# Performance work log

Measured on AMD Instinct MI355X. Metric: run time of the kernel, lower is better.

The kernel has to match this reference:

```python
import jax, jax.numpy as jnp
import numpy as np
from jax import lax

B, Hh, Ww, DIM = 8, 32, 32, 768
NH, NP = 6, 4
DV = int(DIM * 0.5)        # value dim (deform_ratio=0.5) = 384
DH = DV // NH              # per-head dim = 64
HID = int(DIM * 0.25)      # ConvFFN hidden = 192
N_TOK = 21 * (Hh * Ww // 4)  # 5376 query tokens (3-level pyramid)
LIN = Hh * Ww              # 1024 feat tokens (single level)
EPS = 1e-6


def _ln(x, g, b):
    mu = jnp.mean(x, -1, keepdims=True)
    var = jnp.mean((x - mu) ** 2, -1, keepdims=True)
    return (x - mu) * lax.rsqrt(var + EPS) * g + b


def _bilinear(value, loc, h, w):
    # value: (B, h*w, NH, DH); loc: (B, Lq, NH, NP, 2) normalized (x, y) in [0,1]
    # grid_sample semantics: align_corners=False, zero padding
    x = loc[..., 0] * w - 0.5
    y = loc[..., 1] * h - 0.5
    x0 = jnp.floor(x)
    y0 = jnp.floor(y)
    wx = x - x0
    wy = y - y0
    b, lq, nh, p = x.shape
    out = jnp.zeros((b, lq, nh, p, value.shape[-1]), value.dtype)
    for dy, wyy in ((0, 1.0 - wy), (1, wy)):
        for dx, wxx in ((0, 1.0 - wx), (1, wx)):
            xi = x0 + dx
            yi = y0 + dy
            valid = (xi >= 0) & (xi < w) & (yi >= 0) & (yi < h)
            xi_c = jnp.clip(xi, 0, w - 1).astype(jnp.int32)
            yi_c = jnp.clip(yi, 0, h - 1).astype(jnp.int32)
            idx = yi_c * w + xi_c                          # (B,Lq,NH,NP)
            idx = idx.transpose(0, 1, 3, 2).reshape(b, lq * p, nh)
            g = jnp.take_along_axis(value, idx[..., None], axis=1)  # (B,Lq*P,NH,DH)
            g = g.reshape(b, lq, p, nh, -1).transpose(0, 1, 3, 2, 4)
            out = out + g * (wxx * wyy * valid.astype(value.dtype))[..., None]
    return out


def setup_inputs() -> dict:
    key = jax.random.key(0)
    ks = jax.random.split(key, 24)
    s = 0.02
    inp = {
        'query': jax.random.normal(ks[0], (B, N_TOK, DIM), jnp.float32),
        'reference_points': jax.random.uniform(ks[1], (B, N_TOK, 1, 2), jnp.float32),
        'feat': jax.random.normal(ks[2], (B, LIN, DIM), jnp.float32),
        'spatial_shapes': jnp.array([[Hh, Ww]], jnp.int32),
        'level_start_index': jnp.zeros((1,), jnp.int32),
        'qn_g': jnp.ones((DIM,), jnp.float32),
        'qn_b': jnp.zeros((DIM,), jnp.float32),
        'fn_g': jnp.ones((DIM,), jnp.float32),
        'fn_b': jnp.zeros((DIM,), jnp.float32),
        'W_off': jax.random.normal(ks[3], (DIM, NH * NP * 2), jnp.float32) * s,
        'b_off': jax.random.normal(ks[4], (NH * NP * 2,), jnp.float32) * s,
        'W_attn': jax.random.normal(ks[5], (DIM, NH * NP), jnp.float32) * s,
        'b_attn': jnp.zeros((NH * NP,), jnp.float32),
        'W_val': jax.random.normal(ks[6], (DIM, DV), jnp.float32) * s,
        'b_val': jnp.zeros((DV,), jnp.float32),
        'W_out': jax.random.normal(ks[7], (DV, DIM), jnp.float32) * s,
        'b_out': jnp.zeros((DIM,), jnp.float32),
        'ffn_g': jnp.ones((DIM,), jnp.float32),
        'ffn_b': jnp.zeros((DIM,), jnp.float32),
        'fc1_w': jax.random.normal(ks[8], (DIM, HID), jnp.float32) * s,
        'fc1_b': jnp.zeros((HID,), jnp.float32),
        'dw_w': jax.random.normal(ks[9], (3, 3, 1, HID), jnp.float32) * s,  # HWIO depthwise
        'dw_b': jnp.zeros((HID,), jnp.float32),
        'fc2_w': jax.random.normal(ks[10], (HID, DIM), jnp.float32) * s,
        'fc2_b': jnp.zeros((DIM,), jnp.float32),
        'h': Hh,
        'w': Ww,
    }
    return inp


def reference(query, reference_points, feat, spatial_shapes, level_start_index,
              qn_g, qn_b, fn_g, fn_b, W_off, b_off, W_attn, b_attn, W_val, b_val,
              W_out, b_out, ffn_g, ffn_b, fc1_w, fc1_b, dw_w, dw_b, fc2_w, fc2_b,
              h, w):
    b, lq, _ = query.shape
    # ---- MSDeformAttn (single level) ----
    q = _ln(query, qn_g, qn_b)
    v = _ln(feat, fn_g, fn_b) @ W_val + b_val            # (B, LIN, DV)
    v = v.reshape(b, -1, NH, DH)
    off = (q @ W_off + b_off).reshape(b, lq, NH, 1, NP, 2)
    aw = jax.nn.softmax((q @ W_attn + b_attn).reshape(b, lq, NH, NP), axis=-1)
    normalizer = jnp.array([w, h], q.dtype)              # (W, H) for x,y offsets
    loc = reference_points[:, :, None, :, None, :] + off / normalizer  # (B,Lq,NH,1,NP,2)
    sampled = _bilinear(v, loc[:, :, :, 0], h, w)        # (B,Lq,NH,NP,DH)
    attn = jnp.einsum('blhpd,blhp->blhd', sampled, aw).reshape(b, lq, DV)
    attn = attn @ W_out + b_out
    x = query + attn
    # ---- ConvFFN residual ----
    y = _ln(x, ffn_g, ffn_b) @ fc1_w + fc1_b             # (B, N, HID)
    n = lq // 21
    def dw(z, hh, ww):
        z = z.reshape(b, hh, ww, HID)
        z = lax.conv_general_dilated(z, dw_w, (1, 1), 'SAME',
                                     dimension_numbers=('NHWC', 'HWIO', 'NHWC'),
                                     feature_group_count=HID) + dw_b
        return z.reshape(b, hh * ww, HID)
    y = jnp.concatenate([dw(y[:, :16 * n], 2 * h, 2 * w),
                         dw(y[:, 16 * n:20 * n], h, w),
                         dw(y[:, 20 * n:], h // 2, w // 2)], axis=1)
    y = jax.nn.gelu(y, approximate=False)
    y = y @ fc2_w + fc2_b
    return x + y
```

## Files before the change

kernel.cpp:

```cpp
#include <hip/hip_runtime.h>
#include <hip/hip_bf16.h>
#include <math.h>

#define B_    8
#define DIM_  768
#define NH_   6
#define NP_   4
#define DV_   384
#define DH_   64
#define HID_  192
#define NTOK_ 5376
#define LIN_  1024
#define HH_   32
#define WW_   32
#define MQ_   (B_ * NTOK_)
#define MF_   (B_ * LIN_)

using fv4  = __attribute__((ext_vector_type(4))) float;
using bfv8 = __attribute__((ext_vector_type(8))) __bf16;
using sv8  = __attribute__((ext_vector_type(8))) short;
using sv4  = __attribute__((ext_vector_type(4))) short;

__device__ __forceinline__ short f2bf(float f) {
  union { float f; unsigned u; } v; v.f = f;
  unsigned r = v.u + 0x7FFFu + ((v.u >> 16) & 1u);
  return (short)(r >> 16);
}
__device__ __forceinline__ float bf2f(short s) {
  union { unsigned u; float f; } v;
  v.u = ((unsigned)(unsigned short)s) << 16;
  return v.f;
}

__device__ __forceinline__ void gload16(const short* g, short* l) {
  __builtin_amdgcn_global_load_lds(
      (const __attribute__((address_space(1))) void*)g,
      (__attribute__((address_space(3))) void*)l, 16, 0, 0);
}

__device__ __forceinline__ float block_sum_f(float v, float* red, int nwaves) {
#pragma unroll
  for (int o = 32; o > 0; o >>= 1) v += __shfl_down(v, o, 64);
  int wid = threadIdx.x >> 6;
  int lane = threadIdx.x & 63;
  if (lane == 0) red[wid] = v;
  __syncthreads();
  float s = 0.f;
  for (int i = 0; i < nwaves; ++i) s += red[i];
  __syncthreads();
  return s;
}

__global__ __launch_bounds__(256) void ln_apply(const float* __restrict__ X,
                                                const float* __restrict__ g,
                                                const float* __restrict__ b,
                                                short* __restrict__ Y) {
  __shared__ float red[4];
  const int row = blockIdx.x;
  const float* xr = X + (size_t)row * DIM_;
  const int t = threadIdx.x;
  float x0 = xr[t], x1 = xr[t + 256], x2 = xr[t + 512];
  float s = block_sum_f(x0 + x1 + x2, red, 4);
  const float m = s * (1.f / 768.f);
  float d0 = x0 - m, d1 = x1 - m, d2 = x2 - m;
  float sq = block_sum_f(d0 * d0 + d1 * d1 + d2 * d2, red, 4);
  const float rs = rsqrtf(sq * (1.f / 768.f) + 1e-6f);
  short* yr = Y + (size_t)row * DIM_;
  yr[t]       = f2bf(d0 * rs * g[t]       + b[t]);
  yr[t + 256] = f2bf(d1 * rs * g[t + 256] + b[t + 256]);
  yr[t + 512] = f2bf(d2 * rs * g[t + 512] + b[t + 512]);
}

__global__ __launch_bounds__(256) void tconv(const float* __restrict__ src,
                                             short* __restrict__ dst,
                                             int K, int N, int rowOff) {
  const int i = blockIdx.x * 256 + threadIdx.x;
  if (i >= K * N) return;
  const int n = i / K, k = i % K;
  dst[(size_t)(n + rowOff) * K + k] = f2bf(src[(size_t)k * N + n]);
}

__global__ __launch_bounds__(256) void zfill(short* __restrict__ p, int n) {
  const int i = blockIdx.x * 256 + threadIdx.x;
  if (i < n) p[i] = 0;
}

template <int NT>
__global__ __launch_bounds__(256) void gemm_mfma(
    const short* __restrict__ A, const short* __restrict__ Bt,
    const float* __restrict__ bias, const float* __restrict__ addend,
    float* __restrict__ C, short* __restrict__ Cb,
    int M, int N, int K) {
  __shared__ short As[2][8192];
  __shared__ short Bs[2][8192];

  const int bid = blockIdx.x;
  const int xcd = bid & 7;
  const int slot = bid >> 3;
  const int mpx = (M >> 7) >> 3;
  const int mt = xcd * mpx + slot / NT;
  const int nt = slot % NT;
  const int bm = mt << 7;
  const int bn = nt << 7;

  const int t = threadIdx.x;
  const int lane = t & 63;
  const int wid = t >> 6;
  const int wr = (wid >> 1) * 64;
  const int wc = (wid & 1) * 64;
  const int l15 = lane & 15;
  const int l4 = lane >> 4;
  const int lr = lane >> 3;
  const int cs = ((((lane & 7) << 4) ^ (lr << 4)) >> 1);
  const int xorv = (l15 & 7) << 4;

  const short* pa0 = A + (size_t)(bm + wid * 32 + lr) * K + cs;
  const short* pb0 = Bt + (size_t)(bn + wid * 32 + lr) * K + cs;
  short* la0 = &As[0][wid * 2048];
  short* lb0 = &Bs[0][wid * 2048];
  short* la1 = &As[1][wid * 2048];
  short* lb1 = &Bs[1][wid * 2048];

  auto stage = [&](int buf, int kt) {
    const short* pa = pa0 + kt;
    const short* pb = pb0 + kt;
    short* la = buf ? la1 : la0;
    short* lb = buf ? lb1 : lb0;
#pragma unroll
    for (int i = 0; i < 4; ++i) {
      gload16(pa + (size_t)i * 8 * K, la + i * 512);
      gload16(pb + (size_t)i * 8 * K, lb + i * 512);
    }
  };

  fv4 acc[4][4] = {};
  const int nsteps = K >> 6;
  int cur = 0;
  stage(0, 0);
  __syncthreads();

  for (int tstep = 0; tstep < nsteps; ++tstep) {
    if (tstep + 1 < nsteps) stage(cur ^ 1, (tstep + 1) << 6);
    const short* Ab = As[cur];
    const short* Bb = Bs[cur];
#pragma unroll
    for (int kk = 0; kk < 2; ++kk) {
      const int cb = (l4 << 4) + (kk << 6);
      const int co = (cb ^ xorv) >> 1;
      bfv8 af[4], bfr[4];
#pragma unroll
      for (int m = 0; m < 4; ++m)
        af[m] = *(const bfv8*)&Ab[((wr + m * 16 + l15) << 6) + co];
#pragma unroll
      for (int n = 0; n < 4; ++n)
        bfr[n] = *(const bfv8*)&Bb[((wc + n * 16 + l15) << 6) + co];
#pragma unroll
      for (int m = 0; m < 4; ++m)
#pragma unroll
        for (int n = 0; n < 4; ++n)
          acc[m][n] = __builtin_amdgcn_mfma_f32_16x16x32_bf16(
              bfr[n], af[m], acc[m][n], 0, 0, 0);
    }
    __syncthreads();
    cur ^= 1;
  }

  const int rb = bm + wr + l15;
  const int cbase = bn + wc + l4 * 4;
#pragma unroll
  for (int n = 0; n < 4; ++n) {
    const int colb = cbase + n * 16;
    if (colb >= N) continue;
    fv4 bv = {};
    if (bias) bv = *(const fv4*)&bias[colb];
#pragma unroll
    for (int m = 0; m < 4; ++m) {
      const int row = rb + m * 16;
      const size_t o = (size_t)row * N + colb;
      fv4 vv = acc[m][n] + bv;
      if (addend) vv += *(const fv4*)&addend[o];
      if (C) {
        *(fv4*)&C[o] = vv;
      } else {
        sv4 r;
        r[0] = f2bf(vv[0]); r[1] = f2bf(vv[1]);
        r[2] = f2bf(vv[2]); r[3] = f2bf(vv[3]);
        *(sv4*)&Cb[o] = r;
      }
    }
  }
}

__global__ __launch_bounds__(256) void prep_taps(
    const float* __restrict__ ref, const float* __restrict__ boff,
    const float* __restrict__ battn, const float* __restrict__ oa,
    int* __restrict__ taps) {
  const int i = blockIdx.x * 256 + threadIdx.x;
  if (i >= MQ_ * NH_) return;
  const int row = i / NH_, head = i % NH_;
  const float rx = ref[(size_t)row * 2 + 0];
  const float ry = ref[(size_t)row * 2 + 1];
  const float* o = oa + (size_t)row * 72 + head * 8;
  const float* ap = oa + (size_t)row * 72 + 48 + head * 4;
  float l0 = ap[0] + battn[head * 4 + 0];
  float l1 = ap[1] + battn[head * 4 + 1];
  float l2 = ap[2] + battn[head * 4 + 2];
  float l3 = ap[3] + battn[head * 4 + 3];
  float mx = fmaxf(fmaxf(l0, l1), fmaxf(l2, l3));
  float e0 = expf(l0 - mx), e1 = expf(l1 - mx);
  float e2 = expf(l2 - mx), e3 = expf(l3 - mx);
  float sinv = 1.f / (e0 + e1 + e2 + e3);
  float aw[4] = {e0 * sinv, e1 * sinv, e2 * sinv, e3 * sinv};

  int st[32];
  int k = 0;
#pragma unroll
  for (int p = 0; p < 4; ++p) {
    const float lx = rx + (o[p * 2 + 0] + boff[head * 8 + p * 2 + 0]) * (1.f / 32.f);
    const float ly = ry + (o[p * 2 + 1] + boff[head * 8 + p * 2 + 1]) * (1.f / 32.f);
    const float x = lx * (float)WW_ - 0.5f;
    const float y = ly * (float)HH_ - 0.5f;
    const float x0f = floorf(x), y0f = floorf(y);
    const float wx = x - x0f, wy = y - y0f;
    const int x0 = (int)x0f, y0 = (int)y0f;
    const float a = aw[p];
#pragma unroll
    for (int dy = 0; dy < 2; ++dy) {
      const int yi = y0 + dy;
      const float wyy = dy ? wy : 1.f - wy;
#pragma unroll
      for (int dx = 0; dx < 2; ++dx) {
        const int xi = x0 + dx;
        const float wxx = dx ? wx : 1.f - wx;
        const bool valid = ((unsigned)xi < (unsigned)WW_) & ((unsigned)yi < (unsigned)HH_);
        const int xc = min(max(xi, 0), WW_ - 1);
        const int yc = min(max(yi, 0), HH_ - 1);
        st[k++] = (yc * WW_ + xc) * DV_;
        float w = a * wxx * wyy;
        st[k++] = __float_as_int(valid ? w : 0.f);
      }
    }
  }
  int4* dst = (int4*)(taps + (size_t)i * 32);
#pragma unroll
  for (int j = 0; j < 8; ++j)
    dst[j] = make_int4(st[4 * j], st[4 * j + 1], st[4 * j + 2], st[4 * j + 3]);
}

__global__ __launch_bounds__(256) void msda_sample2(const short* __restrict__ v,
                                                    const int* __restrict__ taps,
                                                    short* __restrict__ outv) {
  const int gid = blockIdx.x * 256 + threadIdx.x;
  const int pair = gid >> 4;
  const int ch0 = (gid & 15) * 4;
  const int row = pair / NH_;
  const int head = pair - row * NH_;
  const int b = row / NTOK_;
  const short* vb = v + (size_t)b * LIN_ * DV_ + head * DH_ + ch0;
  const int4* tp = (const int4*)(taps + (size_t)pair * 32);
  float a0 = 0.f, a1 = 0.f, a2 = 0.f, a3 = 0.f;
#pragma unroll
  for (int j = 0; j < 8; ++j) {
    int4 pr = tp[j];
    {
      sv4 val = *(const sv4*)&vb[pr.x];
      const float w = __int_as_float(pr.y);
      a0 += w * bf2f(val[0]); a1 += w * bf2f(val[1]);
      a2 += w * bf2f(val[2]); a3 += w * bf2f(val[3]);
    }
    {
      sv4 val = *(const sv4*)&vb[pr.z];
      const float w = __int_as_float(pr.w);
      a0 += w * bf2f(val[0]); a1 += w * bf2f(val[1]);
      a2 += w * bf2f(val[2]); a3 += w * bf2f(val[3]);
    }
  }
  sv4 r;
  r[0] = f2bf(a0); r[1] = f2bf(a1); r[2] = f2bf(a2); r[3] = f2bf(a3);
  *(sv4*)&outv[(size_t)gid * 4] = r;
}

__global__ __launch_bounds__(256) void conv_gelu(const short* __restrict__ y1,
                                                 const float* __restrict__ dww,
                                                 const float* __restrict__ dwb,
                                                 short* __restrict__ y2) {
  const int i = blockIdx.x * 256 + threadIdx.x;
  if (i >= B_ * NTOK_ * HID_) return;
  const int c = i % HID_;
  const int tmp = i / HID_;
  const int tok = tmp % NTOK_;
  const int b = tmp / NTOK_;
  int base, LH, LW;
  if (tok < 4096)      { base = 0;    LH = 64; LW = 64; }
  else if (tok < 5120) { base = 4096; LH = 32; LW = 32; }
  else                 { base = 5120; LH = 16; LW = 16; }
  const int pos = tok - base;
  const int hh = pos / LW, ww = pos % LW;
  float z = dwb[c];
  const short* yb = y1 + ((size_t)b * NTOK_ + base) * HID_ + c;
#pragma unroll
  for (int ky = 0; ky < 3; ++ky) {
    const int yy = hh + ky - 1;
    if ((unsigned)yy >= (unsigned)LH) continue;
#pragma unroll
    for (int kx = 0; kx < 3; ++kx) {
      const int xx = ww + kx - 1;
      if ((unsigned)xx >= (unsigned)LW) continue;
      z += bf2f(yb[(size_t)(yy * LW + xx) * HID_]) * dww[(ky * 3 + kx) * HID_ + c];
    }
  }
  y2[i] = f2bf(0.5f * z * (1.f + erff(z * 0.70710678118654752f)));
}

extern "C" void kernel_launch(void* const* d_in, const int* in_sizes, int n_in,
                              void* d_out, int out_size, void* d_ws, size_t ws_size,
                              hipStream_t stream) {
  const float* query  = (const float*)d_in[0];
  const float* ref    = (const float*)d_in[1];
  const float* feat   = (const float*)d_in[2];
  const float* qn_g   = (const float*)d_in[5];
  const float* qn_b   = (const float*)d_in[6];
  const float* fn_g   = (const float*)d_in[7];
  const float* fn_b   = (const float*)d_in[8];
  const float* W_off  = (const float*)d_in[9];
  const float* b_off  = (const float*)d_in[10];
  const float* W_attn = (const float*)d_in[11];
  const float* b_attn = (const float*)d_in[12];
  const float* W_val  = (const float*)d_in[13];
  const float* b_val  = (const float*)d_in[14];
  const float* W_out  = (const float*)d_in[15];
  const float* b_out  = (const float*)d_in[16];
  const float* ffn_g  = (const float*)d_in[17];
  const float* ffn_b  = (const float*)d_in[18];
  const float* fc1_w  = (const float*)d_in[19];
  const float* fc1_b  = (const float*)d_in[20];
  const float* dw_w   = (const float*)d_in[21];
  const float* dw_b   = (const float*)d_in[22];
  const float* fc2_w  = (const float*)d_in[23];
  const float* fc2_b  = (const float*)d_in[24];
  float* out = (float*)d_out;
  char* wsb = (char*)d_ws;

  short* qn_xn = (short*)(wsb + 0);
  int*   taps  = (int*)(wsb + 0);
  short* vbf   = (short*)(wsb + 66060288);
  float* oa    = (float*)(wsb + 72351744);
  short* attnv = (short*)(wsb + 84738048);
  short* y1b   = (short*)(wsb + 84738048);
  short* fnb   = (short*)(wsb + 117768192);
  short* y2    = (short*)(wsb + 117768192);
  short* oat   = (short*)(wsb + 130351104);
  short* vt    = (short*)(wsb + 134283264);
  short* ot    = (short*)(wsb + 134873088);
  short* f1t   = (short*)(wsb + 135462912);
  short* f2t   = (short*)(wsb + 135757824);

  zfill<<<(128 * 768 + 255) / 256, 256, 0, stream>>>(oat, 128 * 768);
  tconv<<<(768 * 384 + 255) / 256, 256, 0, stream>>>(W_val, vt, 768, 384, 0);
  tconv<<<(768 * 48 + 255) / 256, 256, 0, stream>>>(W_off, oat, 768, 48, 0);
  tconv<<<(768 * 24 + 255) / 256, 256, 0, stream>>>(W_attn, oat, 768, 24, 48);
  tconv<<<(384 * 768 + 255) / 256, 256, 0, stream>>>(W_out, ot, 384, 768, 0);
  tconv<<<(768 * 192 + 255) / 256, 256, 0, stream>>>(fc1_w, f1t, 768, 192, 0);
  tconv<<<(192 * 768 + 255) / 256, 256, 0, stream>>>(fc2_w, f2t, 192, 768, 0);

  ln_apply<<<MQ_, 256, 0, stream>>>(query, qn_g, qn_b, qn_xn);
  ln_apply<<<MF_, 256, 0, stream>>>(feat, fn_g, fn_b, fnb);

  gemm_mfma<3><<<(MF_ / 128) * 3, 256, 0, stream>>>(
      fnb, vt, b_val, nullptr, nullptr, vbf, MF_, 384, 768);

  gemm_mfma<1><<<(MQ_ / 128) * 1, 256, 0, stream>>>(
      qn_xn, oat, nullptr, nullptr, oa, nullptr, MQ_, 72, 768);

  prep_taps<<<(MQ_ * NH_ + 255) / 256, 256, 0, stream>>>(ref, b_off, b_attn, oa, taps);

  msda_sample2<<<MQ_ * NH_ * 16 / 256, 256, 0, stream>>>(vbf, taps, attnv);

  gemm_mfma<6><<<(MQ_ / 128) * 6, 256, 0, stream>>>(
      attnv, ot, b_out, query, out, nullptr, MQ_, 768, 384);

  ln_apply<<<MQ_, 256, 0, stream>>>(out, ffn_g, ffn_b, qn_xn);

  gemm_mfma<2><<<(MQ_ / 128) * 2, 256, 0, stream>>>(
      qn_xn, f1t, fc1_b, nullptr, nullptr, y1b, MQ_, 192, 768);

  conv_gelu<<<(MQ_ * HID_ + 255) / 256, 256, 0, stream>>>(y1b, dw_w, dw_b, y2);

  gemm_mfma<6><<<(MQ_ / 128) * 6, 256, 0, stream>>>(
      y2, f2t, fc2_b, out, out, nullptr, MQ_, 768, 192);
}
```

Before: 705.7 us.

## Shrink GEMM tiles to 64x64 and vectorize LayerNorm with 192 threads

The MFMA GEMM block tile drops from 128x128 to 64x64, each wave now owning 32x32 with 2x2 accumulators, and the LDS staging is reworked to match. Grids grow roughly fourfold, which raises occupancy and spreads small-N GEMMs over more CUs. The cost is lower arithmetic intensity per block, since each block reloads more A/B data per output. LayerNorm also moves to 192 threads, each loading one float4, storing four bf16 values in one write, and reading gamma and beta as vectors.

```diff
diff --git a/kernel.cpp b/kernel.cpp
--- a/kernel.cpp
+++ b/kernel.cpp
@@ -51,24 +51,28 @@
   return s;
 }
 
-__global__ __launch_bounds__(256) void ln_apply(const float* __restrict__ X,
+__global__ __launch_bounds__(192) void ln_apply(const float* __restrict__ X,
                                                 const float* __restrict__ g,
                                                 const float* __restrict__ b,
                                                 short* __restrict__ Y) {
-  __shared__ float red[4];
+  __shared__ float red[3];
   const int row = blockIdx.x;
-  const float* xr = X + (size_t)row * DIM_;
   const int t = threadIdx.x;
-  float x0 = xr[t], x1 = xr[t + 256], x2 = xr[t + 512];
-  float s = block_sum_f(x0 + x1 + x2, red, 4);
+  const fv4 x = ((const fv4*)(X + (size_t)row * DIM_))[t];
+  float s = block_sum_f(x[0] + x[1] + x[2] + x[3], red, 3);
   const float m = s * (1.f / 768.f);
-  float d0 = x0 - m, d1 = x1 - m, d2 = x2 - m;
-  float sq = block_sum_f(d0 * d0 + d1 * d1 + d2 * d2, red, 4);
+  fv4 d = x - m;
+  float sq = block_sum_f(d[0] * d[0] + d[1] * d[1] + d[2] * d[2] + d[3] * d[3],
+                         red, 3);
   const float rs = rsqrtf(sq * (1.f / 768.f) + 1e-6f);
-  short* yr = Y + (size_t)row * DIM_;
-  yr[t]       = f2bf(d0 * rs * g[t]       + b[t]);
-  yr[t + 256] = f2bf(d1 * rs * g[t + 256] + b[t + 256]);
-  yr[t + 512] = f2bf(d2 * rs * g[t + 512] + b[t + 512]);
+  const fv4 g4 = ((const fv4*)g)[t];
+  const fv4 b4 = ((const fv4*)b)[t];
+  sv4 r;
+  r[0] = f2bf(d[0] * rs * g4[0] + b4[0]);
+  r[1] = f2bf(d[1] * rs * g4[1] + b4[1]);
+  r[2] = f2bf(d[2] * rs * g4[2] + b4[2]);
+  r[3] = f2bf(d[3] * rs * g4[3] + b4[3]);
+  ((sv4*)(Y + (size_t)row * DIM_))[t] = r;
 }
 
 __global__ __launch_bounds__(256) void tconv(const float* __restrict__ src,
@@ -91,49 +95,45 @@
     const float* __restrict__ bias, const float* __restrict__ addend,
     float* __restrict__ C, short* __restrict__ Cb,
     int M, int N, int K) {
-  __shared__ short As[2][8192];
-  __shared__ short Bs[2][8192];
+  __shared__ short As[2][4096];
+  __shared__ short Bs[2][4096];
 
   const int bid = blockIdx.x;
   const int xcd = bid & 7;
   const int slot = bid >> 3;
-  const int mpx = (M >> 7) >> 3;
+  const int mpx = (M >> 6) >> 3;
   const int mt = xcd * mpx + slot / NT;
   const int nt = slot % NT;
-  const int bm = mt << 7;
-  const int bn = nt << 7;
+  const int bm = mt << 6;
+  const int bn = nt << 6;
 
   const int t = threadIdx.x;
   const int lane = t & 63;
   const int wid = t >> 6;
-  const int wr = (wid >> 1) * 64;
-  const int wc = (wid & 1) * 64;
+  const int wr = (wid >> 1) * 32;
+  const int wc = (wid & 1) * 32;
   const int l15 = lane & 15;
   const int l4 = lane >> 4;
   const int lr = lane >> 3;
   const int cs = ((((lane & 7) << 4) ^ (lr << 4)) >> 1);
   const int xorv = (l15 & 7) << 4;
 
-  const short* pa0 = A + (size_t)(bm + wid * 32 + lr) * K + cs;
-  const short* pb0 = Bt + (size_t)(bn + wid * 32 + lr) * K + cs;
-  short* la0 = &As[0][wid * 2048];
-  short* lb0 = &Bs[0][wid * 2048];
-  short* la1 = &As[1][wid * 2048];
-  short* lb1 = &Bs[1][wid * 2048];
+  const short* pa0 = A + (size_t)(bm + wid * 8 + lr) * K + cs;
+  const short* pb0 = Bt + (size_t)(bn + wid * 8 + lr) * K + cs;
 
   auto stage = [&](int buf, int kt) {
     const short* pa = pa0 + kt;
     const short* pb = pb0 + kt;
-    short* la = buf ? la1 : la0;
-    short* lb = buf ? lb1 : lb0;
-#pragma unroll
-    for (int i = 0; i < 4; ++i) {
-      gload16(pa + (size_t)i * 8 * K, la + i * 512);
-      gload16(pb + (size_t)i * 8 * K, lb + i * 512);
+    short* la = &As[buf][wid * 512];
+    short* lb = &Bs[buf][wid * 512];
+#pragma unroll
+    for (int i = 0; i < 2; ++i) {
+      gload16(pa + (size_t)(i * 32) * K, la + i * 2048);
+      gload16(pb + (size_t)(i * 32) * K, lb + i * 2048);
     }
   };
 
-  fv4 acc[4][4] = {};
+  fv4 acc[2][2] = {};
   const int nsteps = K >> 6;
   int cur = 0;
   stage(0, 0);
@@ -147,17 +147,17 @@
     for (int kk = 0; kk < 2; ++kk) {
       const int cb = (l4 << 4) + (kk << 6);
       const int co = (cb ^ xorv) >> 1;
-      bfv8 af[4], bfr[4];
-#pragma unroll
-      for (int m = 0; m < 4; ++m)
+      bfv8 af[2], bfr[2];
+#pragma unroll
+      for (int m = 0; m < 2; ++m)
         af[m] = *(const bfv8*)&Ab[((wr + m * 16 + l15) << 6) + co];
 #pragma unroll
-      for (int n = 0; n < 4; ++n)
+      for (int n = 0; n < 2; ++n)
         bfr[n] = *(const bfv8*)&Bb[((wc + n * 16 + l15) << 6) + co];
 #pragma unroll
-      for (int m = 0; m < 4; ++m)
-#pragma unroll
-        for (int n = 0; n < 4; ++n)
+      for (int m = 0; m < 2; ++m)
+#pragma unroll
+        for (int n = 0; n < 2; ++n)
           acc[m][n] = __builtin_amdgcn_mfma_f32_16x16x32_bf16(
               bfr[n], af[m], acc[m][n], 0, 0, 0);
     }
@@ -168,13 +168,13 @@
   const int rb = bm + wr + l15;
   const int cbase = bn + wc + l4 * 4;
 #pragma unroll
-  for (int n = 0; n < 4; ++n) {
+  for (int n = 0; n < 2; ++n) {
     const int colb = cbase + n * 16;
     if (colb >= N) continue;
     fv4 bv = {};
     if (bias) bv = *(const fv4*)&bias[colb];
 #pragma unroll
-    for (int m = 0; m < 4; ++m) {
+    for (int m = 0; m < 2; ++m) {
       const int row = rb + m * 16;
       const size_t o = (size_t)row * N + colb;
       fv4 vv = acc[m][n] + bv;
@@ -363,29 +363,29 @@
   tconv<<<(768 * 192 + 255) / 256, 256, 0, stream>>>(fc1_w, f1t, 768, 192, 0);
   tconv<<<(192 * 768 + 255) / 256, 256, 0, stream>>>(fc2_w, f2t, 192, 768, 0);
 
-  ln_apply<<<MQ_, 256, 0, stream>>>(query, qn_g, qn_b, qn_xn);
-  ln_apply<<<MF_, 256, 0, stream>>>(feat, fn_g, fn_b, fnb);
-
-  gemm_mfma<3><<<(MF_ / 128) * 3, 256, 0, stream>>>(
+  ln_apply<<<MQ_, 192, 0, stream>>>(query, qn_g, qn_b, qn_xn);
+  ln_apply<<<MF_, 192, 0, stream>>>(feat, fn_g, fn_b, fnb);
+
+  gemm_mfma<6><<<(MF_ / 64) * 6, 256, 0, stream>>>(
       fnb, vt, b_val, nullptr, nullptr, vbf, MF_, 384, 768);
 
-  gemm_mfma<1><<<(MQ_ / 128) * 1, 256, 0, stream>>>(
+  gemm_mfma<2><<<(MQ_ / 64) * 2, 256, 0, stream>>>(
       qn_xn, oat, nullptr, nullptr, oa, nullptr, MQ_, 72, 768);
 
   prep_taps<<<(MQ_ * NH_ + 255) / 256, 256, 0, stream>>>(ref, b_off, b_attn, oa, taps);
 
   msda_sample2<<<MQ_ * NH_ * 16 / 256, 256, 0, stream>>>(vbf, taps, attnv);
 
-  gemm_mfma<6><<<(MQ_ / 128) * 6, 256, 0, stream>>>(
+  gemm_mfma<12><<<(MQ_ / 64) * 12, 256, 0, stream>>>(
       attnv, ot, b_out, query, out, nullptr, MQ_, 768, 384);
 
-  ln_apply<<<MQ_, 256, 0, stream>>>(out, ffn_g, ffn_b, qn_xn);
-
-  gemm_mfma<2><<<(MQ_ / 128) * 2, 256, 0, stream>>>(
+  ln_apply<<<MQ_, 192, 0, stream>>>(out, ffn_g, ffn_b, qn_xn);
+
+  gemm_mfma<3><<<(MQ_ / 64) * 3, 256, 0, stream>>>(
       qn_xn, f1t, fc1_b, nullptr, nullptr, y1b, MQ_, 192, 768);
 
   conv_gelu<<<(MQ_ * HID_ + 255) / 256, 256, 0, stream>>>(y1b, dw_w, dw_b, y2);
 
-  gemm_mfma<6><<<(MQ_ / 128) * 6, 256, 0, stream>>>(
+  gemm_mfma<12><<<(MQ_ / 64) * 12, 256, 0, stream>>>(
       y2, f2t, fc2_b, out, out, nullptr, MQ_, 768, 192);
 }
```

Result: no change. 697.0 us (-1.2%).
